# Optimization experiments

Measured on AMD Instinct MI355X. Metric: run time of the kernel, lower is better.

Reference implementation:

```python
import jax, jax.numpy as jnp
import numpy as np

B, L, D, F = 1, 4096, 4096, 11008
# (start, end, side): side 0 = vision expert, side 1 = language expert.
# Mirrors merge_section_size over alternating contiguous vision/language token ranges.
SEGMENTS = [(0, 1024, 0), (1024, 2048, 1), (2048, 3072, 0), (3072, 4096, 1)]


def setup_inputs() -> dict:
    key = jax.random.key(0)
    ks = jax.random.split(key, 7)
    s = 0.02  # weight init scale
    hidden_states = jax.random.normal(ks[0], (B, L, D), jnp.float32)
    tt = np.zeros((B, L), np.int32)
    for a, b, side in SEGMENTS:
        tt[:, a:b] = side
    token_type_ids = jnp.asarray(tt)
    lg_w = jax.random.normal(ks[1], (D, F), jnp.float32) * s
    lu_w = jax.random.normal(ks[2], (D, F), jnp.float32) * s
    ld_w = jax.random.normal(ks[3], (F, D), jnp.float32) * s
    vg_w = jax.random.normal(ks[4], (D, F), jnp.float32) * s
    vu_w = jax.random.normal(ks[5], (D, F), jnp.float32) * s
    vd_w = jax.random.normal(ks[6], (F, D), jnp.float32) * s
    return {
        'hidden_states': hidden_states,
        'token_type_ids': token_type_ids,
        'lg_w': lg_w, 'lu_w': lu_w, 'ld_w': ld_w,
        'vg_w': vg_w, 'vu_w': vu_w, 'vd_w': vd_w,
    }


def _swiglu_mlp(x, gw, uw, dw):
    # x: [B, T, D] -> [B, T, D]; down(silu(gate(x)) * up(x))
    h = jax.nn.silu(jnp.einsum('btd,df->btf', x, gw)) * jnp.einsum('btd,df->btf', x, uw)
    return jnp.einsum('btf,fd->btd', h, dw)


def reference(hidden_states, token_type_ids, lg_w, lu_w, ld_w, vg_w, vu_w, vd_w):
    # Split-dispatch over static contiguous segments, then concat along seq dim.
    outs = []
    for a, b, side in SEGMENTS:
        seg = hidden_states[:, a:b, :]
        if side == 1:
            outs.append(_swiglu_mlp(seg, lg_w, lu_w, ld_w))
        else:
            outs.append(_swiglu_mlp(seg, vg_w, vu_w, vd_w))
    return jnp.concatenate(outs, axis=1)
```

## Files before the change

kernel.cpp:

```cpp
#include <hip/hip_runtime.h>
#include <math.h>

typedef unsigned short u16;
typedef short s16x8 __attribute__((ext_vector_type(8)));
typedef float f32x4 __attribute__((ext_vector_type(4)));

#define GLOAD16(gp, lp)                                                        \
  __builtin_amdgcn_global_load_lds(                                            \
      (const __attribute__((address_space(1))) void*)(gp),                     \
      (__attribute__((address_space(3))) void*)(lp), 16, 0, 0)

__device__ __forceinline__ u16 f2bf(float f) {
  union { float f; unsigned u; } v; v.f = f;
  unsigned r = v.u + 0x7fffu + ((v.u >> 16) & 1u);
  return (u16)(r >> 16);
}

__global__ __launch_bounds__(256) void prep_kernel(
    const float* __restrict__ in0, const float* __restrict__ in1,
    const float* __restrict__ in2, const float* __restrict__ in3,
    const float* __restrict__ in4, const float* __restrict__ in5,
    const float* __restrict__ xin,
    u16* __restrict__ o01, u16* __restrict__ o23,
    u16* __restrict__ o4, u16* __restrict__ o5, u16* __restrict__ xout) {
  const int mat = blockIdx.y;
  const int t = threadIdx.x;
  if (mat == 6) {
    if (blockIdx.x >= 8192) return;
    size_t i = ((size_t)blockIdx.x * 256 + t) * 8;
    float4 a = *(const float4*)(xin + i);
    float4 b = *(const float4*)(xin + i + 4);
    s16x8 v;
    v[0] = (short)f2bf(a.x); v[1] = (short)f2bf(a.y);
    v[2] = (short)f2bf(a.z); v[3] = (short)f2bf(a.w);
    v[4] = (short)f2bf(b.x); v[5] = (short)f2bf(b.y);
    v[6] = (short)f2bf(b.z); v[7] = (short)f2bf(b.w);
    *(s16x8*)(xout + i) = v;
    return;
  }
  __shared__ float s[64 * 65];
  const float* in; u16* out;
  switch (mat) {
    case 0: in = in0; out = o01; break;
    case 1: in = in1; out = o01; break;
    case 2: in = in2; out = o23; break;
    case 3: in = in3; out = o23; break;
    case 4: in = in4; out = o4; break;
    default: in = in5; out = o5; break;
  }
  const int R = (mat < 4) ? 4096 : 11008;
  const int C = (mat < 4) ? 11008 : 4096;
  const int nTc = C >> 6;
  const int tr = blockIdx.x / nTc, tc = blockIdx.x - tr * nTc;
  const int r0 = tr << 6, c0 = tc << 6;
#pragma unroll
  for (int p = 0; p < 4; ++p) {
    const int lr = p * 16 + (t >> 4);
    const int lc = (t & 15) * 4;
    float4 v = *(const float4*)(in + (size_t)(r0 + lr) * C + (c0 + lc));
    float* sp = &s[lr * 65 + lc];
    sp[0] = v.x; sp[1] = v.y; sp[2] = v.z; sp[3] = v.w;
  }
  __syncthreads();
#pragma unroll
  for (int q = 0; q < 2; ++q) {
    const int oc = q * 32 + (t >> 3);
    const int orr = (t & 7) * 8;
    s16x8 v;
#pragma unroll
    for (int i = 0; i < 8; ++i) v[i] = (short)f2bf(s[(orr + i) * 65 + oc]);
    const int f = c0 + oc;
    size_t orow;
    if (mat < 4) orow = (size_t)((f >> 4) << 5) + ((mat & 1) << 4) + (f & 15);
    else         orow = (size_t)f;
    *(s16x8*)(out + orow * R + (r0 + orr)) = v;
  }
}

#define SBAR() __builtin_amdgcn_s_barrier()
#define LGKM0() asm volatile("s_waitcnt lgkmcnt(0)")
#define LGKM8() asm volatile("s_waitcnt lgkmcnt(8)")
#define VMCNT6() asm volatile("s_waitcnt vmcnt(6)")
#define VMCNT0() asm volatile("s_waitcnt vmcnt(0)")

__global__ __launch_bounds__(512, 1) void gemm_gateup_queue(
    const u16* __restrict__ A, const u16* __restrict__ Bl,
    const u16* __restrict__ Bv, const int* __restrict__ tt,
    u16* __restrict__ H, int* __restrict__ qcnt) {
  __shared__ u16 sA[2][2][128][64];
  __shared__ u16 sB[2][2][128][64];
  __shared__ int sQ;

  const int t = threadIdx.x;
  const int lane = t & 63;
  const int rlo = lane & 15;
  const int hi = lane >> 4;
  const int wn = (t >> 6) & 3;
  const int wm = (t >> 8) & 1;

  const int rowq = t >> 3;
  const int gsw = ((t & 7) ^ (rowq & 7)) << 4;
  char* ldsA = (char*)&sA[0][0][0][0];
  char* ldsB = (char*)&sB[0][0][0][0];
  const int woff = (t & 448) << 4;

  const int cxa = (hi ^ (rlo & 7)) << 4;
  const int cxb = ((4 + hi) ^ (rlo & 7)) << 4;
  const int arow = (wm * 64 + rlo) * 128;
  const int brow = (wn * 32 + rlo) * 128;

  s16x8 af[4][2], bf[2][2][2];
  f32x4 acc[8][4];
  const f32x4 z = {0.f, 0.f, 0.f, 0.f};

#define QSTG_A(d, h, kt)                                                       \
  do {                                                                         \
    GLOAD16(srcA + (size_t)((h) * 128) * 8192 + (kt) * 128,                    \
            ldsA + (d) * 32768 + (h) * 16384 + woff);                          \
    GLOAD16(srcA + (size_t)((h) * 128 + 64) * 8192 + (kt) * 128,               \
            ldsA + (d) * 32768 + (h) * 16384 + 8192 + woff);                   \
  } while (0)
#define QSTG_B(d, h, kt)                                                       \
  do {                                                                         \
    GLOAD16(srcB + (size_t)((h) * 128) * 8192 + (kt) * 128,                    \
            ldsB + (d) * 32768 + (h) * 16384 + woff);                          \
    GLOAD16(srcB + (size_t)((h) * 128 + 64) * 8192 + (kt) * 128,               \
            ldsB + (d) * 32768 + (h) * 16384 + 8192 + woff);                   \
  } while (0)
#define LDA(d, mh)                                                             \
  do {                                                                         \
    _Pragma("unroll") for (int fi = 0; fi < 4; ++fi) {                         \
      const char* p = ldsA + (d) * 32768 + (mh) * 16384 + arow + fi * 2048;    \
      af[fi][0] = *(const s16x8*)(p + cxa);                                    \
      af[fi][1] = *(const s16x8*)(p + cxb);                                    \
    }                                                                          \
  } while (0)
#define LDBS(bi, d, nh)                                                        \
  do {                                                                         \
    _Pragma("unroll") for (int gi = 0; gi < 2; ++gi) {                         \
      const char* p = ldsB + (d) * 32768 + (nh) * 16384 + brow + gi * 2048;    \
      bf[bi][gi][0] = *(const s16x8*)(p + cxa);                                \
      bf[bi][gi][1] = *(const s16x8*)(p + cxb);                                \
    }                                                                          \
  } while (0)
#define MFMA16(mh, nh)                                                         \
  do {                                                                         \
    __builtin_amdgcn_s_setprio(1);                                             \
    _Pragma("unroll") for (int fi = 0; fi < 4; ++fi)                           \
        _Pragma("unroll") for (int gi = 0; gi < 2; ++gi) {                     \
      acc[(mh)*4 + fi][(nh)*2 + gi] = __builtin_amdgcn_mfma_f32_16x16x32_bf16( \
          af[fi][0], bf[nh][gi][0], acc[(mh)*4 + fi][(nh)*2 + gi], 0, 0, 0);   \
      acc[(mh)*4 + fi][(nh)*2 + gi] = __builtin_amdgcn_mfma_f32_16x16x32_bf16( \
          af[fi][1], bf[nh][gi][1], acc[(mh)*4 + fi][(nh)*2 + gi], 0, 0, 0);   \
    }                                                                          \
    __builtin_amdgcn_s_setprio(0);                                             \
  } while (0)

  for (;;) {
    __syncthreads();
    if (t == 0) sQ = atomicAdd(qcnt, 1);
    __syncthreads();
    const int q = sQ;
    if (q >= 1376) break;
    const int nT = q >> 4;
    const int mT = q & 15;
    const int side = tt[mT << 8];
    const u16* GU = side ? Bl : Bv;
    const char* srcA = (const char*)A + (size_t)(mT * 256 + rowq) * 8192 + gsw;
    const char* srcB = (const char*)GU + (size_t)(nT * 256 + rowq) * 8192 + gsw;

#pragma unroll
    for (int i = 0; i < 8; ++i)
#pragma unroll
      for (int j = 0; j < 4; ++j) acc[i][j] = z;

    QSTG_A(0, 0, 0); QSTG_B(0, 0, 0); QSTG_B(0, 1, 0); QSTG_A(0, 1, 0);
    QSTG_A(1, 0, 1); QSTG_B(1, 0, 1); QSTG_B(1, 1, 1);
    VMCNT6();
    SBAR();

    for (int T = 0; T < 62; T += 2) {
      LDA(0, 0); LDBS(0, 0, 0);
      QSTG_A(1, 1, T + 1);
      LGKM8();
      SBAR(); LGKM0(); MFMA16(0, 0); SBAR();
      LDBS(1, 0, 1);
      QSTG_A(0, 0, T + 2);
      SBAR(); LGKM0(); MFMA16(0, 1); SBAR();
      LDA(0, 1);
      QSTG_B(0, 0, T + 2);
      SBAR(); LGKM0(); MFMA16(1, 1); SBAR();
      QSTG_B(0, 1, T + 2);
      VMCNT6();
      SBAR(); MFMA16(1, 0); SBAR();
      LDA(1, 0); LDBS(0, 1, 0);
      QSTG_A(0, 1, T + 2);
      LGKM8();
      SBAR(); LGKM0(); MFMA16(0, 0); SBAR();
      LDBS(1, 1, 1);
      QSTG_A(1, 0, T + 3);
      SBAR(); LGKM0(); MFMA16(0, 1); SBAR();
      LDA(1, 1);
      QSTG_B(1, 0, T + 3);
      SBAR(); LGKM0(); MFMA16(1, 1); SBAR();
      QSTG_B(1, 1, T + 3);
      VMCNT6();
      SBAR(); MFMA16(1, 0); SBAR();
    }
    {
      LDA(0, 0); LDBS(0, 0, 0);
      QSTG_A(1, 1, 63);
      LGKM8();
      SBAR(); LGKM0(); MFMA16(0, 0); SBAR();
      LDBS(1, 0, 1);
      SBAR(); LGKM0(); MFMA16(0, 1); SBAR();
      LDA(0, 1);
      SBAR(); LGKM0(); MFMA16(1, 1); SBAR();
      VMCNT0();
      SBAR(); MFMA16(1, 0); SBAR();
      LDA(1, 0); LDBS(0, 1, 0);
      LGKM8();
      SBAR(); LGKM0(); MFMA16(0, 0); SBAR();
      LDBS(1, 1, 1);
      SBAR(); LGKM0(); MFMA16(0, 1); SBAR();
      LDA(1, 1);
      SBAR(); LGKM0(); MFMA16(1, 1); SBAR();
      MFMA16(1, 0);
    }

#pragma unroll
    for (int mh = 0; mh < 2; ++mh)
#pragma unroll
      for (int fi = 0; fi < 4; ++fi) {
        const int row0 = mT * 256 + mh * 128 + wm * 64 + fi * 16 + hi * 4;
#pragma unroll
        for (int nh = 0; nh < 2; ++nh) {
          const int fc = nT * 128 + (nh * 4 + wn) * 16 + rlo;
          const f32x4 g = acc[mh * 4 + fi][nh * 2 + 0];
          const f32x4 u = acc[mh * 4 + fi][nh * 2 + 1];
#pragma unroll
          for (int r = 0; r < 4; ++r) {
            const float gv = g[r];
            const float hv = gv / (1.f + __expf(-gv)) * u[r];
            H[(size_t)(row0 + r) * 11008 + fc] = f2bf(hv);
          }
        }
      }
  }
#undef QSTG_A
#undef QSTG_B
#undef LDA
#undef LDBS
#undef MFMA16
}

__global__ __launch_bounds__(512, 1) void gemm_down(
    const u16* __restrict__ A, const u16* __restrict__ Bl,
    const u16* __restrict__ Bv, const int* __restrict__ tt,
    float* __restrict__ O) {
  constexpr int KB = 22016;
  constexpr int NK = KB / 128;
  __shared__ u16 sA[2][2][128][64];
  __shared__ u16 sB[2][2][128][64];

  const int bid = blockIdx.x;
  const int wg = (bid & 7) * 32 + (bid >> 3);
  const int mT = wg & 15;
  const int nT = wg >> 4;

  const int t = threadIdx.x;
  const int lane = t & 63;
  const int rlo = lane & 15;
  const int hi = lane >> 4;
  const int wn = (t >> 6) & 3;
  const int wm = (t >> 8) & 1;

  const int side = tt[mT << 8];
  const u16* B = side ? Bl : Bv;

  const int rowq = t >> 3;
  const int gsw = ((t & 7) ^ (rowq & 7)) << 4;
  const char* srcA = (const char*)A + (size_t)(mT * 256 + rowq) * KB + gsw;
  const char* srcB = (const char*)B + (size_t)(nT * 256 + rowq) * KB + gsw;
  char* ldsA = (char*)&sA[0][0][0][0];
  char* ldsB = (char*)&sB[0][0][0][0];
  const int woff = (t & 448) << 4;

#define STG_A(d, h, kt)                                                        \
  do {                                                                         \
    GLOAD16(srcA + (size_t)((h) * 128) * KB + (kt) * 128,                      \
            ldsA + (d) * 32768 + (h) * 16384 + woff);                          \
    GLOAD16(srcA + (size_t)((h) * 128 + 64) * KB + (kt) * 128,                 \
            ldsA + (d) * 32768 + (h) * 16384 + 8192 + woff);                   \
  } while (0)
#define STG_B(d, h, kt)                                                        \
  do {                                                                         \
    GLOAD16(srcB + (size_t)((h) * 128) * KB + (kt) * 128,                      \
            ldsB + (d) * 32768 + (h) * 16384 + woff);                          \
    GLOAD16(srcB + (size_t)((h) * 128 + 64) * KB + (kt) * 128,                 \
            ldsB + (d) * 32768 + (h) * 16384 + 8192 + woff);                   \
  } while (0)

  const int cxa = (hi ^ (rlo & 7)) << 4;
  const int cxb = ((4 + hi) ^ (rlo & 7)) << 4;
  const int arow = (wm * 64 + rlo) * 128;
  const int brow = (wn * 32 + rlo) * 128;

  s16x8 af[4][2], bf[2][2][2];
  f32x4 acc[8][4];
  const f32x4 z = {0.f, 0.f, 0.f, 0.f};
#pragma unroll
  for (int i = 0; i < 8; ++i)
#pragma unroll
    for (int j = 0; j < 4; ++j) acc[i][j] = z;

#define LDA(d, mh)                                                             \
  do {                                                                         \
    _Pragma("unroll") for (int fi = 0; fi < 4; ++fi) {                         \
      const char* p = ldsA + (d) * 32768 + (mh) * 16384 + arow + fi * 2048;    \
      af[fi][0] = *(const s16x8*)(p + cxa);                                    \
      af[fi][1] = *(const s16x8*)(p + cxb);                                    \
    }                                                                          \
  } while (0)
#define LDBS(bi, d, nh)                                                        \
  do {                                                                         \
    _Pragma("unroll") for (int gi = 0; gi < 2; ++gi) {                         \
      const char* p = ldsB + (d) * 32768 + (nh) * 16384 + brow + gi * 2048;    \
      bf[bi][gi][0] = *(const s16x8*)(p + cxa);                                \
      bf[bi][gi][1] = *(const s16x8*)(p + cxb);                                \
    }                                                                          \
  } while (0)
#define MFMA16(mh, nh)                                                         \
  do {                                                                         \
    __builtin_amdgcn_s_setprio(1);                                             \
    _Pragma("unroll") for (int fi = 0; fi < 4; ++fi)                           \
        _Pragma("unroll") for (int gi = 0; gi < 2; ++gi) {                     \
      acc[(mh)*4 + fi][(nh)*2 + gi] = __builtin_amdgcn_mfma_f32_16x16x32_bf16( \
          af[fi][0], bf[nh][gi][0], acc[(mh)*4 + fi][(nh)*2 + gi], 0, 0, 0);   \
      acc[(mh)*4 + fi][(nh)*2 + gi] = __builtin_amdgcn_mfma_f32_16x16x32_bf16( \
          af[fi][1], bf[nh][gi][1], acc[(mh)*4 + fi][(nh)*2 + gi], 0, 0, 0);   \
    }                                                                          \
    __builtin_amdgcn_s_setprio(0);                                             \
  } while (0)

  STG_A(0, 0, 0); STG_B(0, 0, 0); STG_B(0, 1, 0); STG_A(0, 1, 0);
  STG_A(1, 0, 1); STG_B(1, 0, 1); STG_B(1, 1, 1);
  VMCNT6();
  SBAR();

  for (int T = 0; T < NK - 2; T += 2) {
    LDA(0, 0); LDBS(0, 0, 0);
    STG_A(1, 1, T + 1);
    LGKM8();
    SBAR(); LGKM0(); MFMA16(0, 0); SBAR();
    LDBS(1, 0, 1);
    STG_A(0, 0, T + 2);
    SBAR(); LGKM0(); MFMA16(0, 1); SBAR();
    LDA(0, 1);
    STG_B(0, 0, T + 2);
    SBAR(); LGKM0(); MFMA16(1, 1); SBAR();
    STG_B(0, 1, T + 2);
    VMCNT6();
    SBAR(); MFMA16(1, 0); SBAR();
    LDA(1, 0); LDBS(0, 1, 0);
    STG_A(0, 1, T + 2);
    LGKM8();
    SBAR(); LGKM0(); MFMA16(0, 0); SBAR();
    LDBS(1, 1, 1);
    STG_A(1, 0, T + 3);
    SBAR(); LGKM0(); MFMA16(0, 1); SBAR();
    LDA(1, 1);
    STG_B(1, 0, T + 3);
    SBAR(); LGKM0(); MFMA16(1, 1); SBAR();
    STG_B(1, 1, T + 3);
    VMCNT6();
    SBAR(); MFMA16(1, 0); SBAR();
  }
  {
    LDA(0, 0); LDBS(0, 0, 0);
    STG_A(1, 1, NK - 1);
    LGKM8();
    SBAR(); LGKM0(); MFMA16(0, 0); SBAR();
    LDBS(1, 0, 1);
    SBAR(); LGKM0(); MFMA16(0, 1); SBAR();
    LDA(0, 1);
    SBAR(); LGKM0(); MFMA16(1, 1); SBAR();
    VMCNT0();
    SBAR(); MFMA16(1, 0); SBAR();
    LDA(1, 0); LDBS(0, 1, 0);
    LGKM8();
    SBAR(); LGKM0(); MFMA16(0, 0); SBAR();
    LDBS(1, 1, 1);
    SBAR(); LGKM0(); MFMA16(0, 1); SBAR();
    LDA(1, 1);
    SBAR(); LGKM0(); MFMA16(1, 1); SBAR();
    MFMA16(1, 0);
  }

#pragma unroll
  for (int mh = 0; mh < 2; ++mh)
#pragma unroll
    for (int fi = 0; fi < 4; ++fi) {
      const int row0 = mT * 256 + mh * 128 + wm * 64 + fi * 16 + hi * 4;
#pragma unroll
      for (int nh = 0; nh < 2; ++nh)
#pragma unroll
        for (int gi = 0; gi < 2; ++gi) {
          const int col = nT * 256 + nh * 128 + wn * 32 + gi * 16 + rlo;
          const f32x4 a = acc[mh * 4 + fi][nh * 2 + gi];
#pragma unroll
          for (int r = 0; r < 4; ++r)
            O[(size_t)(row0 + r) * 4096 + col] = a[r];
        }
    }
#undef STG_A
#undef STG_B
#undef LDA
#undef LDBS
#undef MFMA16
}

extern "C" void kernel_launch(void* const* d_in, const int* in_sizes, int n_in,
                              void* d_out, int out_size, void* d_ws, size_t ws_size,
                              hipStream_t stream) {
  (void)in_sizes; (void)n_in; (void)out_size; (void)ws_size;
  const float* x  = (const float*)d_in[0];
  const int*   tt = (const int*)d_in[1];
  const float* lg = (const float*)d_in[2];
  const float* lu = (const float*)d_in[3];
  const float* ld = (const float*)d_in[4];
  const float* vg = (const float*)d_in[5];
  const float* vu = (const float*)d_in[6];
  const float* vd = (const float*)d_in[7];

  u16* ws  = (u16*)d_ws;
  u16* xbf = ws;
  u16* GUl = xbf + 16777216;
  u16* GUv = GUl + 90177536;
  u16* ldT = GUv + 90177536;
  u16* vdT = ldT + 45088768;
  u16* hbuf = vdT + 45088768;
  int* qcnt = (int*)(hbuf + 45088768);

  hipMemsetAsync(qcnt, 0, 4, stream);
  prep_kernel<<<dim3(11008, 7), dim3(256), 0, stream>>>(
      lg, lu, vg, vu, ld, vd, x, GUl, GUv, ldT, vdT, xbf);
  gemm_gateup_queue<<<dim3(256), dim3(512), 0, stream>>>(
      xbf, GUl, GUv, tt, hbuf, qcnt);
  gemm_down<<<dim3(256), dim3(512), 0, stream>>>(hbuf, ldT, vdT, tt, (float*)d_out);
}
```

Baseline: 1.314 ms.

## Rework gate/up GEMM to BK=32 triple-buffered 256x128 tiles with two blocks per CU

The gate/up GEMM tile shrinks from 256x256 with K-step 64 (double buffered) to 256x128 with K-step 32 and a three-stage LDS ring. LDS use and register pressure drop so two 512-thread blocks can share a CU, and the grid and queue length double to 512 blocks and 2752 tiles. The aim is better latency hiding and occupancy. In exchange each loaded tile is reused less, there are more barriers per unit of K, and the A operand is fetched again for each narrower N tile.

```diff
diff --git a/kernel.cpp b/kernel.cpp
--- a/kernel.cpp
+++ b/kernel.cpp
@@ -81,14 +81,15 @@
 #define LGKM0() asm volatile("s_waitcnt lgkmcnt(0)")
 #define LGKM8() asm volatile("s_waitcnt lgkmcnt(8)")
 #define VMCNT6() asm volatile("s_waitcnt vmcnt(6)")
+#define VMCNT3() asm volatile("s_waitcnt vmcnt(3)")
 #define VMCNT0() asm volatile("s_waitcnt vmcnt(0)")
 
-__global__ __launch_bounds__(512, 1) void gemm_gateup_queue(
+__global__ __launch_bounds__(512, 4) void gemm_gateup_bk32(
     const u16* __restrict__ A, const u16* __restrict__ Bl,
     const u16* __restrict__ Bv, const int* __restrict__ tt,
     u16* __restrict__ H, int* __restrict__ qcnt) {
-  __shared__ u16 sA[2][2][128][64];
-  __shared__ u16 sB[2][2][128][64];
+  __shared__ u16 sA[3][2][128][32];
+  __shared__ u16 sB[3][128][32];
   __shared__ int sQ;
 
   const int t = threadIdx.x;
@@ -98,61 +99,44 @@
   const int wn = (t >> 6) & 3;
   const int wm = (t >> 8) & 1;
 
-  const int rowq = t >> 3;
-  const int gsw = ((t & 7) ^ (rowq & 7)) << 4;
+  const int rowq = t >> 2;
+  const int gsw = ((t & 3) ^ ((rowq >> 1) & 3)) << 4;
   char* ldsA = (char*)&sA[0][0][0][0];
-  char* ldsB = (char*)&sB[0][0][0][0];
-  const int woff = (t & 448) << 4;
-
-  const int cxa = (hi ^ (rlo & 7)) << 4;
-  const int cxb = ((4 + hi) ^ (rlo & 7)) << 4;
-  const int arow = (wm * 64 + rlo) * 128;
-  const int brow = (wn * 32 + rlo) * 128;
-
-  s16x8 af[4][2], bf[2][2][2];
-  f32x4 acc[8][4];
+  char* ldsB = (char*)&sB[0][0][0];
+  const int woff = (t >> 6) << 10;
+
+  const int cx = (hi ^ ((rlo >> 1) & 3)) << 4;
+  const int aoff = wm * 8192 + rlo * 64 + cx;
+  const int boff = wn * 2048 + rlo * 64 + cx;
+
+  s16x8 af[4], bf[2];
+  f32x4 acc[8][2];
   const f32x4 z = {0.f, 0.f, 0.f, 0.f};
 
-#define QSTG_A(d, h, kt)                                                       \
-  do {                                                                         \
-    GLOAD16(srcA + (size_t)((h) * 128) * 8192 + (kt) * 128,                    \
-            ldsA + (d) * 32768 + (h) * 16384 + woff);                          \
-    GLOAD16(srcA + (size_t)((h) * 128 + 64) * 8192 + (kt) * 128,               \
-            ldsA + (d) * 32768 + (h) * 16384 + 8192 + woff);                   \
-  } while (0)
-#define QSTG_B(d, h, kt)                                                       \
-  do {                                                                         \
-    GLOAD16(srcB + (size_t)((h) * 128) * 8192 + (kt) * 128,                    \
-            ldsB + (d) * 32768 + (h) * 16384 + woff);                          \
-    GLOAD16(srcB + (size_t)((h) * 128 + 64) * 8192 + (kt) * 128,               \
-            ldsB + (d) * 32768 + (h) * 16384 + 8192 + woff);                   \
-  } while (0)
-#define LDA(d, mh)                                                             \
-  do {                                                                         \
-    _Pragma("unroll") for (int fi = 0; fi < 4; ++fi) {                         \
-      const char* p = ldsA + (d) * 32768 + (mh) * 16384 + arow + fi * 2048;    \
-      af[fi][0] = *(const s16x8*)(p + cxa);                                    \
-      af[fi][1] = *(const s16x8*)(p + cxb);                                    \
-    }                                                                          \
-  } while (0)
-#define LDBS(bi, d, nh)                                                        \
-  do {                                                                         \
-    _Pragma("unroll") for (int gi = 0; gi < 2; ++gi) {                         \
-      const char* p = ldsB + (d) * 32768 + (nh) * 16384 + brow + gi * 2048;    \
-      bf[bi][gi][0] = *(const s16x8*)(p + cxa);                                \
-      bf[bi][gi][1] = *(const s16x8*)(p + cxb);                                \
-    }                                                                          \
-  } while (0)
-#define MFMA16(mh, nh)                                                         \
+#define GSTG(bv, kt)                                                           \
+  do {                                                                         \
+    GLOAD16(srcA + (kt) * 64, ldsA + (bv) * 16384 + woff);                     \
+    GLOAD16(srcA + 1048576 + (kt) * 64, ldsA + (bv) * 16384 + 8192 + woff);    \
+    GLOAD16(srcB + (kt) * 64, ldsB + (bv) * 8192 + woff);                      \
+  } while (0)
+#define GLDA(bv, mh)                                                           \
+  do {                                                                         \
+    _Pragma("unroll") for (int fi = 0; fi < 4; ++fi)                           \
+        af[fi] = *(const s16x8*)(ldsA + (bv) * 16384 + aoff +                  \
+                                 (mh) * 4096 + fi * 1024);                     \
+  } while (0)
+#define GLDB(bv)                                                               \
+  do {                                                                         \
+    bf[0] = *(const s16x8*)(ldsB + (bv) * 8192 + boff);                        \
+    bf[1] = *(const s16x8*)(ldsB + (bv) * 8192 + boff + 1024);                 \
+  } while (0)
+#define GMFMA(mh)                                                              \
   do {                                                                         \
     __builtin_amdgcn_s_setprio(1);                                             \
     _Pragma("unroll") for (int fi = 0; fi < 4; ++fi)                           \
-        _Pragma("unroll") for (int gi = 0; gi < 2; ++gi) {                     \
-      acc[(mh)*4 + fi][(nh)*2 + gi] = __builtin_amdgcn_mfma_f32_16x16x32_bf16( \
-          af[fi][0], bf[nh][gi][0], acc[(mh)*4 + fi][(nh)*2 + gi], 0, 0, 0);   \
-      acc[(mh)*4 + fi][(nh)*2 + gi] = __builtin_amdgcn_mfma_f32_16x16x32_bf16( \
-          af[fi][1], bf[nh][gi][1], acc[(mh)*4 + fi][(nh)*2 + gi], 0, 0, 0);   \
-    }                                                                          \
+        _Pragma("unroll") for (int gi = 0; gi < 2; ++gi)                       \
+        acc[(mh)*4 + fi][gi] = __builtin_amdgcn_mfma_f32_16x16x32_bf16(        \
+            af[fi], bf[gi], acc[(mh)*4 + fi][gi], 0, 0, 0);                    \
     __builtin_amdgcn_s_setprio(0);                                             \
   } while (0)
 
@@ -161,97 +145,59 @@
     if (t == 0) sQ = atomicAdd(qcnt, 1);
     __syncthreads();
     const int q = sQ;
-    if (q >= 1376) break;
+    if (q >= 2752) break;
     const int nT = q >> 4;
     const int mT = q & 15;
     const int side = tt[mT << 8];
     const u16* GU = side ? Bl : Bv;
     const char* srcA = (const char*)A + (size_t)(mT * 256 + rowq) * 8192 + gsw;
-    const char* srcB = (const char*)GU + (size_t)(nT * 256 + rowq) * 8192 + gsw;
-
-#pragma unroll
-    for (int i = 0; i < 8; ++i)
-#pragma unroll
-      for (int j = 0; j < 4; ++j) acc[i][j] = z;
-
-    QSTG_A(0, 0, 0); QSTG_B(0, 0, 0); QSTG_B(0, 1, 0); QSTG_A(0, 1, 0);
-    QSTG_A(1, 0, 1); QSTG_B(1, 0, 1); QSTG_B(1, 1, 1);
-    VMCNT6();
+    const char* srcB = (const char*)GU + (size_t)(nT * 128 + rowq) * 8192 + gsw;
+
+#pragma unroll
+    for (int i = 0; i < 8; ++i) { acc[i][0] = z; acc[i][1] = z; }
+
+    GSTG(0, 0); GSTG(1, 1);
+    VMCNT3();
     SBAR();
 
-    for (int T = 0; T < 62; T += 2) {
-      LDA(0, 0); LDBS(0, 0, 0);
-      QSTG_A(1, 1, T + 1);
-      LGKM8();
-      SBAR(); LGKM0(); MFMA16(0, 0); SBAR();
-      LDBS(1, 0, 1);
-      QSTG_A(0, 0, T + 2);
-      SBAR(); LGKM0(); MFMA16(0, 1); SBAR();
-      LDA(0, 1);
-      QSTG_B(0, 0, T + 2);
-      SBAR(); LGKM0(); MFMA16(1, 1); SBAR();
-      QSTG_B(0, 1, T + 2);
-      VMCNT6();
-      SBAR(); MFMA16(1, 0); SBAR();
-      LDA(1, 0); LDBS(0, 1, 0);
-      QSTG_A(0, 1, T + 2);
-      LGKM8();
-      SBAR(); LGKM0(); MFMA16(0, 0); SBAR();
-      LDBS(1, 1, 1);
-      QSTG_A(1, 0, T + 3);
-      SBAR(); LGKM0(); MFMA16(0, 1); SBAR();
-      LDA(1, 1);
-      QSTG_B(1, 0, T + 3);
-      SBAR(); LGKM0(); MFMA16(1, 1); SBAR();
-      QSTG_B(1, 1, T + 3);
-      VMCNT6();
-      SBAR(); MFMA16(1, 0); SBAR();
+    int b = 0, b2 = 2;
+    for (int T = 0; T < 126; ++T) {
+      GLDA(b, 0); GLDB(b);
+      GSTG(b2, T + 2);
+      SBAR(); LGKM0(); GMFMA(0); SBAR();
+      GLDA(b, 1);
+      SBAR(); LGKM0(); GMFMA(1);
+      VMCNT3(); SBAR();
+      b = (b == 2) ? 0 : b + 1;
+      b2 = (b2 == 2) ? 0 : b2 + 1;
     }
-    {
-      LDA(0, 0); LDBS(0, 0, 0);
-      QSTG_A(1, 1, 63);
-      LGKM8();
-      SBAR(); LGKM0(); MFMA16(0, 0); SBAR();
-      LDBS(1, 0, 1);
-      SBAR(); LGKM0(); MFMA16(0, 1); SBAR();
-      LDA(0, 1);
-      SBAR(); LGKM0(); MFMA16(1, 1); SBAR();
-      VMCNT0();
-      SBAR(); MFMA16(1, 0); SBAR();
-      LDA(1, 0); LDBS(0, 1, 0);
-      LGKM8();
-      SBAR(); LGKM0(); MFMA16(0, 0); SBAR();
-      LDBS(1, 1, 1);
-      SBAR(); LGKM0(); MFMA16(0, 1); SBAR();
-      LDA(1, 1);
-      SBAR(); LGKM0(); MFMA16(1, 1); SBAR();
-      MFMA16(1, 0);
+    GLDA(0, 0); GLDB(0);
+    SBAR(); LGKM0(); GMFMA(0); SBAR();
+    GLDA(0, 1);
+    SBAR(); LGKM0(); GMFMA(1);
+    VMCNT0(); SBAR();
+    GLDA(1, 0); GLDB(1);
+    SBAR(); LGKM0(); GMFMA(0); SBAR();
+    GLDA(1, 1);
+    SBAR(); LGKM0(); GMFMA(1);
+
+    const int f = nT * 64 + wn * 16 + rlo;
+#pragma unroll
+    for (int fi = 0; fi < 8; ++fi) {
+      const int row0 = mT * 256 + wm * 128 + fi * 16 + hi * 4;
+#pragma unroll
+      for (int r = 0; r < 4; ++r) {
+        const float gv = acc[fi][0][r];
+        const float uv = acc[fi][1][r];
+        const float hv = gv / (1.f + __expf(-gv)) * uv;
+        H[(size_t)(row0 + r) * 11008 + f] = f2bf(hv);
+      }
     }
-
-#pragma unroll
-    for (int mh = 0; mh < 2; ++mh)
-#pragma unroll
-      for (int fi = 0; fi < 4; ++fi) {
-        const int row0 = mT * 256 + mh * 128 + wm * 64 + fi * 16 + hi * 4;
-#pragma unroll
-        for (int nh = 0; nh < 2; ++nh) {
-          const int fc = nT * 128 + (nh * 4 + wn) * 16 + rlo;
-          const f32x4 g = acc[mh * 4 + fi][nh * 2 + 0];
-          const f32x4 u = acc[mh * 4 + fi][nh * 2 + 1];
-#pragma unroll
-          for (int r = 0; r < 4; ++r) {
-            const float gv = g[r];
-            const float hv = gv / (1.f + __expf(-gv)) * u[r];
-            H[(size_t)(row0 + r) * 11008 + fc] = f2bf(hv);
-          }
-        }
-      }
-  }
-#undef QSTG_A
-#undef QSTG_B
-#undef LDA
-#undef LDBS
-#undef MFMA16
+  }
+#undef GSTG
+#undef GLDA
+#undef GLDB
+#undef GMFMA
 }
 
 __global__ __launch_bounds__(512, 1) void gemm_down(
@@ -442,10 +388,10 @@
   u16* hbuf = vdT + 45088768;
   int* qcnt = (int*)(hbuf + 45088768);
 
-  hipMemsetAsync(qcnt, 0, 4, stream);
+  (void)hipMemsetAsync(qcnt, 0, 4, stream);
   prep_kernel<<<dim3(11008, 7), dim3(256), 0, stream>>>(
       lg, lu, vg, vu, ld, vd, x, GUl, GUv, ldT, vdT, xbf);
-  gemm_gateup_queue<<<dim3(256), dim3(512), 0, stream>>>(
+  gemm_gateup_bk32<<<dim3(512), dim3(512), 0, stream>>>(
       xbf, GUl, GUv, tt, hbuf, qcnt);
   gemm_down<<<dim3(256), dim3(512), 0, stream>>>(hbuf, ldT, vdT, tt, (float*)d_out);
 }
```

Result: slower. 1.457 ms (+10.9%).
